# Kernel tuning notes

Measured on AMD Instinct MI355X. Metric: run time of the kernel, lower is better.

Reference implementation:

```python
import jax, jax.numpy as jnp
import numpy as np
from jax import lax


def _compute_Bp(lam):
    # Bʹ[k, j] = 1 / prod_{i != j} (1 - λ_i / λ_j), via log-sum for stability.
    k, n = lam.shape
    ratios = lam[:, :, None] / lam[:, None, :]           # [k, n, n], entry (i, j) = λ_i / λ_j
    eye = jnp.eye(n, dtype=bool)[None]                    # zero out diagonal (log(1-0)=0)
    ratios = jnp.where(eye, jnp.zeros((), ratios.dtype), ratios)
    lnBp = -jnp.sum(jnp.log(1.0 - ratios), axis=1)        # [k, n]
    return jnp.exp(lnBp)


def _linear_recurrence(a, b):
    # s_t = a_t * s_{t-1} + b_t (elementwise, diagonal), parallel associative scan over time.
    def combine(c1, c2):
        a1, b1 = c1
        a2, b2 = c2
        return a1 * a2, b1 * a2 + b2
    return lax.associative_scan(combine, (a, b), axis=0)[1]


def _ldstack_forward(x, R, theta, lnC_r, lnC_i, D, Do):
    b, T, d = x.shape
    k, half_n = theta.shape
    n = 2 * half_n
    m = D.shape[1]

    # average=True path: project d -> k, go time-major, lift to complex
    xp = jnp.einsum('btd,dk->btk', x, R)
    xc = jnp.transpose(xp, (1, 0, 2)).astype(jnp.complex64)      # [T, b, k]

    # unitary_constitute: λ = exp(i * [θ, -θ]) on the unit circle
    lam = jnp.exp(jnp.concatenate([theta, -theta], axis=1) * 1j)  # [k, n] complex64
    Cp = jnp.exp(lnC_r + 1j * lnC_i)                              # [k, n, m] complex64

    Bp = _compute_Bp(lam)                                         # [k, n]
    Bx = xc[..., None] * Bp                                       # [T, b, k, n]
    al = jnp.broadcast_to(lam, (T, b, k, n))                      # α is None for Δ=1

    # standard=True: shift coefficients one step (state lags input)
    zeros = jnp.zeros((1, b, k, n), dtype=jnp.complex64)
    al = jnp.concatenate([zeros, al[:-1]], axis=0)
    Bx = jnp.concatenate([zeros, Bx[:-1]], axis=0)

    s = _linear_recurrence(al, Bx)                                # [T, b, k, n]

    Cs = jnp.einsum('tbkn,knm->tbkm', s, Cp)                      # readout
    Dx = xc[..., None] * D.astype(jnp.complex64)[None, None]      # [T, b, k, m]
    y = Cs + Dx + Do.astype(jnp.complex64)                        # [T, b, k, m]

    y = jnp.mean(y, axis=2)                                       # average over k
    y = jnp.real(y)                                               # [T, b, m]
    return jnp.transpose(y, (1, 0, 2))                            # [b, T, m]


def setup_inputs() -> dict:
    b, T, d = 8, 2048, 128
    k, n, m = 32, 32, 128
    key = jax.random.key(0)
    ks = jax.random.split(key, 7)
    x = jax.random.normal(ks[0], (b, T, d), dtype=jnp.float32)
    R = jax.random.normal(ks[1], (d, k), dtype=jnp.float32)
    theta = jax.random.uniform(ks[2], (k, n // 2), dtype=jnp.float32,
                               minval=-np.pi, maxval=np.pi)
    lnC_r = 1e-4 * jax.random.normal(ks[3], (k, n, m), dtype=jnp.float32)
    lnC_i = 1e-4 * jax.random.normal(ks[4], (k, n, m), dtype=jnp.float32)
    D = jax.random.uniform(ks[5], (k, m), dtype=jnp.float32, minval=-1e-3, maxval=1e-3)
    Do = jax.random.uniform(ks[6], (m,), dtype=jnp.float32, minval=-1e-7, maxval=1e-7)
    return {"x": x, "R": R, "theta": theta, "lnC_r": lnC_r, "lnC_i": lnC_i,
            "D": D, "Do": Do}


def reference(x, R, theta, lnC_r, lnC_i, D, Do):
    return _ldstack_forward(x, R, theta, lnC_r, lnC_i, D, Do)
```

## Files before the change

kernel.cpp:

```cpp
#include <hip/hip_runtime.h>
#include <hip/hip_bf16.h>
#include <math.h>

#define K_  32
#define HN  16
#define N_  32
#define M_  128
#define B_  8
#define T_  2048
#define D_  128
#define BT  (B_*T_)
#define KA  1056
#define CHK 32
#define CL  64
#define NSER (B_*K_*HN)
#define NSC  (NSER*CHK)

typedef short short8 __attribute__((ext_vector_type(8)));
typedef float floatx4 __attribute__((ext_vector_type(4)));
typedef unsigned short ushort_t;
typedef unsigned int uint_t;

__device__ __forceinline__ ushort_t f2bf(float f) {
    __hip_bfloat16 h = __float2bfloat16(f);
    return *reinterpret_cast<ushort_t*>(&h);
}
__device__ __forceinline__ uint_t pack_bf2(float re, float im) {
    return ((uint_t)f2bf(im) << 16) | (uint_t)f2bf(re);
}

__global__ __launch_bounds__(256) void k_pre(const float* __restrict__ theta,
                                             const float* __restrict__ lnC_r,
                                             const float* __restrict__ lnC_i,
                                             const float* __restrict__ D,
                                             const float* __restrict__ x,
                                             const float* __restrict__ R,
                                             float* __restrict__ ws,
                                             ushort_t* __restrict__ Wt,
                                             float* __restrict__ xpT,
                                             ushort_t* __restrict__ A2) {
    __shared__ float xls[32 * 128];
    int bid = blockIdx.x, tid = threadIdx.x;
    if (bid == 0) {
        #pragma unroll
        for (int rep = 0; rep < 2; ++rep) {
            int t2 = rep * 256 + tid;
            int k = t2 >> 4, j = t2 & 15;
            float angj = theta[k * HN + j];
            float pr = 1.f, pi = 0.f;
            for (int i = 0; i < N_; ++i) {
                if (i == j) continue;
                float angi = (i < HN) ? theta[k * HN + i] : -theta[k * HN + i - HN];
                float d = angi - angj;
                float tr = 1.f - cosf(d);
                float ti = -sinf(d);
                float nr = pr * tr - pi * ti;
                float ni = pr * ti + pi * tr;
                pr = nr; pi = ni;
            }
            float den = pr * pr + pi * pi;
            ws[t2]        = cosf(angj);
            ws[512 + t2]  = sinf(angj);
            ws[1024 + t2] = pr / den;
            ws[1536 + t2] = -pi / den;
        }
    } else if (bid <= 272) {
        int t = (bid - 1) * 256 + tid;
        const float inv = 1.f / 32.f;
        if (t < K_ * HN * M_) {
            int m = t & 127, j = (t >> 7) & 15, k = t >> 11;
            int i0 = (k * N_ + j) * M_ + m;
            int i1 = (k * N_ + j + HN) * M_ + m;
            float r0 = expf(lnC_r[i0]), c0 = cosf(lnC_i[i0]), s0 = sinf(lnC_i[i0]);
            float r1 = expf(lnC_r[i1]), c1 = cosf(lnC_i[i1]), s1 = sinf(lnC_i[i1]);
            float wr = (r0 * c0 + r1 * c1) * inv;
            float wi = (r1 * s1 - r0 * s0) * inv;
            *(uint_t*)(Wt + (size_t)m * KA + k * 32 + 2 * j) = pack_bf2(wr, wi);
        } else if (t < K_ * HN * M_ + K_ * M_) {
            int u = t - K_ * HN * M_;
            int m = u & 127, k = u >> 7;
            Wt[(size_t)m * KA + 1024 + k] = f2bf(D[k * M_ + m] * inv);
        }
    } else {
        int xb = bid - 273;
        int b = xb >> 6;
        int tbase = (xb & 63) * 32;
        const float4* xsrc = (const float4*)(x + ((size_t)b * T_ + tbase) * D_);
        float4* xd = (float4*)xls;
        #pragma unroll
        for (int e = 0; e < 4; ++e) xd[tid + 256 * e] = xsrc[tid + 256 * e];
        __syncthreads();
        int kk = tid & 31, rg = tid >> 5;
        float accv[4] = {0.f, 0.f, 0.f, 0.f};
        #pragma unroll 4
        for (int i = 0; i < D_; ++i) {
            float rv = R[i * K_ + kk];
            #pragma unroll
            for (int rr = 0; rr < 4; ++rr)
                accv[rr] += xls[(rg + 8 * rr) * D_ + i] * rv;
        }
        #pragma unroll
        for (int rr = 0; rr < 4; ++rr) {
            int tt = tbase + rg + 8 * rr;
            A2[(size_t)(tt * 8 + b) * KA + 1024 + kk] = f2bf(accv[rr]);
            size_t base = (size_t)(b * K_ + kk) * T_;
            if (tt < T_ - 1) xpT[base + tt + 1] = accv[rr];
            if (tt == 0)     xpT[base] = 0.f;
        }
    }
}

__global__ __launch_bounds__(256) void k_scan_ends(const float* __restrict__ xpT,
                                                   const float* __restrict__ ws,
                                                   float* __restrict__ E) {
    int gid = blockIdx.x * 256 + threadIdx.x;
    int j = gid & 15, c = (gid >> 4) & 31, k = (gid >> 9) & 31, b = gid >> 14;
    int col = k * 16 + j;
    float lr = ws[col], li = ws[512 + col], br = ws[1024 + col], bi = ws[1536 + col];
    float sr = 0.f, si = 0.f;
    const float4* xv4 = (const float4*)(xpT + (size_t)(b * K_ + k) * T_ + c * CL);
    for (int u = 0; u < CL / 4; ++u) {
        float4 xv = xv4[u];
        #pragma unroll
        for (int v = 0; v < 4; ++v) {
            float x1 = (v == 0) ? xv.x : (v == 1) ? xv.y : (v == 2) ? xv.z : xv.w;
            float nr = br * x1 + lr * sr - li * si;
            float ni = bi * x1 + lr * si + li * sr;
            sr = nr; si = ni;
        }
    }
    size_t eidx = ((size_t)(b * 32 + k) * 32 + c) * 16 + j;
    E[eidx] = sr;
    E[NSC + eidx] = si;
}

__global__ void k_carries(const float* __restrict__ ws,
                          const float* __restrict__ E,
                          float* __restrict__ S) {
    int tid = blockIdx.x * blockDim.x + threadIdx.x;
    int j = tid & 15, k = (tid >> 4) & 31, b = tid >> 9;
    int col = k * 16 + j;
    float lr = ws[col], li = ws[512 + col];
    float pr = lr, pi = li;
    #pragma unroll
    for (int q = 0; q < 6; ++q) {
        float nr = pr * pr - pi * pi;
        float ni = 2.f * pr * pi;
        pr = nr; pi = ni;
    }
    float sr = 0.f, si = 0.f;
    size_t base = (size_t)(b * 32 + k) * 32 * 16 + j;
    for (int c = 0; c < CHK; ++c) {
        size_t idx = base + (size_t)c * 16;
        S[idx] = sr;
        S[NSC + idx] = si;
        float er = E[idx], ei = E[NSC + idx];
        float nr = pr * sr - pi * si + er;
        float ni = pr * si + pi * sr + ei;
        sr = nr; si = ni;
    }
}

__global__ __launch_bounds__(256) void k_scan_write(const float* __restrict__ xpT,
                                                    const float* __restrict__ ws,
                                                    const float* __restrict__ S,
                                                    uint_t* __restrict__ A2u) {
    int gid = blockIdx.x * 256 + threadIdx.x;
    int j = gid & 15, c = (gid >> 4) & 31, k = (gid >> 9) & 31, b = gid >> 14;
    int col = k * 16 + j;
    float lr = ws[col], li = ws[512 + col], br = ws[1024 + col], bi = ws[1536 + col];
    size_t sidx = ((size_t)(b * 32 + k) * 32 + c) * 16 + j;
    float sr = S[sidx], si = S[NSC + sidx];
    int t0 = c * CL;
    const float4* xv4 = (const float4*)(xpT + (size_t)(b * K_ + k) * T_ + t0);
    uint_t* Ab = A2u + (size_t)(t0 * 8 + b) * (KA / 2) + col;
    for (int u = 0; u < CL / 4; ++u) {
        float4 xv = xv4[u];
        #pragma unroll
        for (int v = 0; v < 4; ++v) {
            float x1 = (v == 0) ? xv.x : (v == 1) ? xv.y : (v == 2) ? xv.z : xv.w;
            float nr = br * x1 + lr * sr - li * si;
            float ni = bi * x1 + lr * si + li * sr;
            sr = nr; si = ni;
            Ab[0] = pack_bf2(sr, si);
            Ab += 8 * (KA / 2);
        }
    }
}

__global__ __launch_bounds__(256, 2) void k_gemm(const ushort_t* __restrict__ A2,
                                                 const ushort_t* __restrict__ Wt,
                                                 const float* __restrict__ Do,
                                                 float* __restrict__ out) {
    int tid = threadIdx.x;
    int wave = tid >> 6;
    int rh = wave & 1;
    int chh = wave >> 1;
    int lane = tid & 63;
    int l16 = lane & 15;
    int quad = lane >> 4;
    int row0 = blockIdx.x * 32 + rh * 16;

    const ushort_t* Ap = A2 + (size_t)(row0 + l16) * KA + quad * 8;
    const ushort_t* Wp = Wt + (size_t)(chh * 64 + l16) * KA + quad * 8;

    floatx4 acc[4];
    #pragma unroll
    for (int n = 0; n < 4; ++n) acc[n] = (floatx4){0.f, 0.f, 0.f, 0.f};

    for (int g = 0; g < 11; ++g) {
        int k0 = g * 96;
        short8 a0 = *(const short8*)(Ap + k0);
        short8 a1 = *(const short8*)(Ap + k0 + 32);
        short8 a2 = *(const short8*)(Ap + k0 + 64);
        short8 bv[4][3];
        #pragma unroll
        for (int n = 0; n < 4; ++n) {
            #pragma unroll
            for (int s = 0; s < 3; ++s)
                bv[n][s] = *(const short8*)(Wp + (size_t)n * 16 * KA + k0 + s * 32);
        }
        #pragma unroll
        for (int n = 0; n < 4; ++n)
            acc[n] = __builtin_amdgcn_mfma_f32_16x16x32_bf16(a0, bv[n][0], acc[n], 0, 0, 0);
        #pragma unroll
        for (int n = 0; n < 4; ++n)
            acc[n] = __builtin_amdgcn_mfma_f32_16x16x32_bf16(a1, bv[n][1], acc[n], 0, 0, 0);
        #pragma unroll
        for (int n = 0; n < 4; ++n)
            acc[n] = __builtin_amdgcn_mfma_f32_16x16x32_bf16(a2, bv[n][2], acc[n], 0, 0, 0);
    }

    #pragma unroll
    for (int n = 0; n < 4; ++n) {
        int col = chh * 64 + n * 16 + l16;
        float dov = Do[col];
        #pragma unroll
        for (int q = 0; q < 4; ++q) {
            int r = row0 + quad * 4 + q;
            int b = r & 7, t = r >> 3;
            out[(size_t)(b * T_ + t) * M_ + col] = acc[n][q] + dov;
        }
    }
}

extern "C" void kernel_launch(void* const* d_in, const int* in_sizes, int n_in,
                              void* d_out, int out_size, void* d_ws, size_t ws_size,
                              hipStream_t stream) {
    const float* x     = (const float*)d_in[0];
    const float* R     = (const float*)d_in[1];
    const float* theta = (const float*)d_in[2];
    const float* lnC_r = (const float*)d_in[3];
    const float* lnC_i = (const float*)d_in[4];
    const float* D     = (const float*)d_in[5];
    const float* Do    = (const float*)d_in[6];
    float* out = (float*)d_out;

    float* wsf   = (float*)d_ws;
    float* lambp = wsf;
    ushort_t* Wt = (ushort_t*)(wsf + 2048);
    ushort_t* A2 = (ushort_t*)(wsf + 2048 + 67584);
    float* xpT   = wsf + 2048 + 67584 + 8650752;
    float* E     = xpT + (size_t)BT * K_;
    float* S     = E + 2 * (size_t)NSC;

    k_pre<<<785, 256, 0, stream>>>(theta, lnC_r, lnC_i, D, x, R,
                                   lambp, Wt, xpT, A2);
    k_scan_ends<<<NSC / 256, 256, 0, stream>>>(xpT, lambp, E);
    k_carries<<<16, 256, 0, stream>>>(lambp, E, S);
    k_scan_write<<<NSC / 256, 256, 0, stream>>>(xpT, lambp, S, (uint_t*)A2);
    k_gemm<<<512, 256, 0, stream>>>(A2, Wt, Do, out);
}
```

Measured before the change: 132.6 us.

## Fuse three-pass chunked scan into one kernel with shared-memory carries

Replaces the chunk-end scan, carry propagation and scan-write kernels with a single kernel per (batch, k) block. The block stages the projected input series in shared memory, computes chunk end states, runs the serial carry pass on 16 threads, then re-scans and writes bf16 states. This removes two launches and the global round trips for the end and carry buffers. The cost is a serial carry phase with most threads idle and only 256 blocks of 512 threads to fill the device.

```diff
diff --git a/kernel.cpp b/kernel.cpp
--- a/kernel.cpp
+++ b/kernel.cpp
@@ -13,8 +13,6 @@
 #define KA  1056
 #define CHK 32
 #define CL  64
-#define NSER (B_*K_*HN)
-#define NSC  (NSER*CHK)
 
 typedef short short8 __attribute__((ext_vector_type(8)));
 typedef float floatx4 __attribute__((ext_vector_type(4)));
@@ -110,75 +108,66 @@
     }
 }
 
-__global__ __launch_bounds__(256) void k_scan_ends(const float* __restrict__ xpT,
-                                                   const float* __restrict__ ws,
-                                                   float* __restrict__ E) {
-    int gid = blockIdx.x * 256 + threadIdx.x;
-    int j = gid & 15, c = (gid >> 4) & 31, k = (gid >> 9) & 31, b = gid >> 14;
+__global__ __launch_bounds__(512) void k_scan(const float* __restrict__ xpT,
+                                              const float* __restrict__ ws,
+                                              uint_t* __restrict__ A2u) {
+    __shared__ float xls[T_];
+    __shared__ float Er[512], Ei[512];
+
+    int tid = threadIdx.x;
+    int k = blockIdx.x & 31, b = blockIdx.x >> 5;
+    int c = tid >> 4, j = tid & 15;
     int col = k * 16 + j;
-    float lr = ws[col], li = ws[512 + col], br = ws[1024 + col], bi = ws[1536 + col];
-    float sr = 0.f, si = 0.f;
-    const float4* xv4 = (const float4*)(xpT + (size_t)(b * K_ + k) * T_ + c * CL);
-    for (int u = 0; u < CL / 4; ++u) {
-        float4 xv = xv4[u];
-        #pragma unroll
-        for (int v = 0; v < 4; ++v) {
-            float x1 = (v == 0) ? xv.x : (v == 1) ? xv.y : (v == 2) ? xv.z : xv.w;
+
+    ((float4*)xls)[tid] = ((const float4*)(xpT + (size_t)(b * K_ + k) * T_))[tid];
+    __syncthreads();
+
+    float lr = ws[col], li = ws[512 + col];
+    float br = ws[1024 + col], bi = ws[1536 + col];
+
+    {
+        float sr = 0.f, si = 0.f;
+        const float* xc = xls + c * CL;
+        #pragma unroll 4
+        for (int p = 0; p < CL; ++p) {
+            float x1 = xc[p];
             float nr = br * x1 + lr * sr - li * si;
             float ni = bi * x1 + lr * si + li * sr;
             sr = nr; si = ni;
         }
-    }
-    size_t eidx = ((size_t)(b * 32 + k) * 32 + c) * 16 + j;
-    E[eidx] = sr;
-    E[NSC + eidx] = si;
-}
-
-__global__ void k_carries(const float* __restrict__ ws,
-                          const float* __restrict__ E,
-                          float* __restrict__ S) {
-    int tid = blockIdx.x * blockDim.x + threadIdx.x;
-    int j = tid & 15, k = (tid >> 4) & 31, b = tid >> 9;
-    int col = k * 16 + j;
-    float lr = ws[col], li = ws[512 + col];
-    float pr = lr, pi = li;
-    #pragma unroll
-    for (int q = 0; q < 6; ++q) {
-        float nr = pr * pr - pi * pi;
-        float ni = 2.f * pr * pi;
-        pr = nr; pi = ni;
-    }
-    float sr = 0.f, si = 0.f;
-    size_t base = (size_t)(b * 32 + k) * 32 * 16 + j;
-    for (int c = 0; c < CHK; ++c) {
-        size_t idx = base + (size_t)c * 16;
-        S[idx] = sr;
-        S[NSC + idx] = si;
-        float er = E[idx], ei = E[NSC + idx];
-        float nr = pr * sr - pi * si + er;
-        float ni = pr * si + pi * sr + ei;
-        sr = nr; si = ni;
-    }
-}
-
-__global__ __launch_bounds__(256) void k_scan_write(const float* __restrict__ xpT,
-                                                    const float* __restrict__ ws,
-                                                    const float* __restrict__ S,
-                                                    uint_t* __restrict__ A2u) {
-    int gid = blockIdx.x * 256 + threadIdx.x;
-    int j = gid & 15, c = (gid >> 4) & 31, k = (gid >> 9) & 31, b = gid >> 14;
-    int col = k * 16 + j;
-    float lr = ws[col], li = ws[512 + col], br = ws[1024 + col], bi = ws[1536 + col];
-    size_t sidx = ((size_t)(b * 32 + k) * 32 + c) * 16 + j;
-    float sr = S[sidx], si = S[NSC + sidx];
-    int t0 = c * CL;
-    const float4* xv4 = (const float4*)(xpT + (size_t)(b * K_ + k) * T_ + t0);
-    uint_t* Ab = A2u + (size_t)(t0 * 8 + b) * (KA / 2) + col;
-    for (int u = 0; u < CL / 4; ++u) {
-        float4 xv = xv4[u];
-        #pragma unroll
-        for (int v = 0; v < 4; ++v) {
-            float x1 = (v == 0) ? xv.x : (v == 1) ? xv.y : (v == 2) ? xv.z : xv.w;
+        Er[c * 16 + j] = sr;
+        Ei[c * 16 + j] = si;
+    }
+    __syncthreads();
+
+    if (tid < 16) {
+        float pr = lr, pi = li;
+        #pragma unroll
+        for (int q = 0; q < 6; ++q) {
+            float nr = pr * pr - pi * pi;
+            float ni = 2.f * pr * pi;
+            pr = nr; pi = ni;
+        }
+        float sr = 0.f, si = 0.f;
+        for (int cc = 0; cc < CHK; ++cc) {
+            int idx = cc * 16 + tid;
+            float er = Er[idx], ei = Ei[idx];
+            Er[idx] = sr; Ei[idx] = si;
+            float nr = pr * sr - pi * si + er;
+            float ni = pr * si + pi * sr + ei;
+            sr = nr; si = ni;
+        }
+    }
+    __syncthreads();
+
+    {
+        float sr = Er[c * 16 + j], si = Ei[c * 16 + j];
+        int t0 = c * CL;
+        const float* xc = xls + t0;
+        uint_t* Ab = A2u + (size_t)(t0 * 8 + b) * (KA / 2) + col;
+        #pragma unroll 4
+        for (int p = 0; p < CL; ++p) {
+            float x1 = xc[p];
             float nr = br * x1 + lr * sr - li * si;
             float ni = bi * x1 + lr * si + li * sr;
             sr = nr; si = ni;
@@ -261,13 +250,9 @@
     ushort_t* Wt = (ushort_t*)(wsf + 2048);
     ushort_t* A2 = (ushort_t*)(wsf + 2048 + 67584);
     float* xpT   = wsf + 2048 + 67584 + 8650752;
-    float* E     = xpT + (size_t)BT * K_;
-    float* S     = E + 2 * (size_t)NSC;
 
     k_pre<<<785, 256, 0, stream>>>(theta, lnC_r, lnC_i, D, x, R,
                                    lambp, Wt, xpT, A2);
-    k_scan_ends<<<NSC / 256, 256, 0, stream>>>(xpT, lambp, E);
-    k_carries<<<16, 256, 0, stream>>>(lambp, E, S);
-    k_scan_write<<<NSC / 256, 256, 0, stream>>>(xpT, lambp, S, (uint_t*)A2);
+    k_scan<<<256, 512, 0, stream>>>(xpT, lambp, (uint_t*)A2);
     k_gemm<<<512, 256, 0, stream>>>(A2, Wt, Do, out);
 }
```

Result: faster. 127.1 us (-4.1%).
